# Kernel optimization log

Measured on AMD Instinct MI355X. Metric: run time of the kernel, lower is better.

## Reference

```python
import jax, jax.numpy as jnp
import numpy as np

B, T, D_IN, HID, D_OUT = 16, 4096, 256, 512, 256


def setup_inputs() -> dict:
    key = jax.random.key(0)
    k0, k1, k2, k3 = jax.random.split(key, 4)
    x = jax.random.normal(k0, (B, T, D_IN), dtype=jnp.float32)
    # nn.Linear default init ~ U(-1/sqrt(fan_in), 1/sqrt(fan_in)); approximate with scaled normal
    W_in = jax.random.normal(k1, (HID, D_IN), dtype=jnp.float32) / np.sqrt(D_IN)
    # hidden_ff.weight is explicitly set to diag(rand(hid_dim)) in the module
    W_h = jnp.diag(jax.random.uniform(k2, (HID,), dtype=jnp.float32))
    W_out = jax.random.normal(k3, (D_OUT, HID), dtype=jnp.float32) / np.sqrt(HID)
    return {"x": x, "W_in": W_in, "W_h": W_h, "W_out": W_out}


def reference(x, W_in, W_h, W_out):
    # x: [B, T, D_in]; W_in: [H, D_in]; W_h: [H, H]; W_out: [D_out, H]
    xp = jnp.einsum('btd,hd->bth', x, W_in)  # input projection, [B, T, H]

    def step(h, xt):
        # h_t = x_t + h_{t-1} @ W_h^T  (linear recurrence, h_0 = 0)
        h_next = xt + h @ W_h.T
        return h_next, h_next

    h0 = jnp.zeros((x.shape[0], W_h.shape[0]), dtype=x.dtype)
    _, hs = jax.lax.scan(step, h0, jnp.swapaxes(xp, 0, 1))  # hs: [T, B, H]
    hs = jnp.swapaxes(hs, 0, 1)  # [B, T, H]
    return jnp.einsum('bth,oh->bto', hs, W_out)  # [B, T, D_out]
```

## Files before the change

kernel.cpp:

```cpp
#include <hip/hip_runtime.h>
#include <hip/hip_bf16.h>
#include <stdint.h>

#define BATCH 16
#define SEQT  4096
#define DIN   256
#define HID   512
#define DOUT  256
#define M_TOT 65536
#define CLEN  128
#define NCHUNK 32

typedef short bf16x8 __attribute__((ext_vector_type(8)));
typedef float f32x4  __attribute__((ext_vector_type(4)));
typedef unsigned short u16;
typedef unsigned short u16x4 __attribute__((ext_vector_type(4)));
typedef unsigned int uint32;

__device__ __forceinline__ void ld_lds16(const void* g, void* l) {
    __builtin_amdgcn_global_load_lds(
        (const __attribute__((address_space(1))) void*)g,
        (__attribute__((address_space(3))) void*)l, 16, 0, 0);
}

__device__ __forceinline__ u16 f2bf_rne(float f) {
    uint32 v = __float_as_uint(f);
    v += 0x7FFFu + ((v >> 16) & 1u);
    return (u16)(v >> 16);
}

__device__ __forceinline__ void splitf(float f, u16& hi, u16& lo) {
    const uint32 u = __float_as_uint(f);
    hi = (u16)(u >> 16);
    lo = f2bf_rne(f - __uint_as_float(u & 0xFFFF0000u));
}

__global__ __launch_bounds__(256) void prep(
        const float* __restrict__ Wh, const float* __restrict__ Win,
        const float* __restrict__ Wout, float* __restrict__ wdiag,
        float* __restrict__ wpow, u16* __restrict__ Winhi,
        u16* __restrict__ Winlo, u16* __restrict__ Wouthi,
        u16* __restrict__ Woutlo) {
    const int bid = blockIdx.x, tid = threadIdx.x;
    if (bid == 0) {
        for (int h = tid; h < HID; h += 256) {
            const float wv = Wh[(size_t)h * HID + h];
            wdiag[h] = wv;
            float p = 1.f;
            for (int t = 0; t < CLEN; ++t) { p *= wv; wpow[t * HID + h] = p; }
        }
    } else if (bid <= 128) {
        const int f4 = (bid - 1) * 256 + tid;
        const f32x4 v = *(const f32x4*)(Win + (size_t)f4 * 4);
        u16x4 hv, lv;
#pragma unroll
        for (int k = 0; k < 4; ++k) { u16 a, b; splitf(v[k], a, b); hv[k] = a; lv[k] = b; }
        *(u16x4*)(Winhi + (size_t)f4 * 4) = hv;
        *(u16x4*)(Winlo + (size_t)f4 * 4) = lv;
    } else {
        const int f4 = (bid - 129) * 256 + tid;
        const f32x4 v = *(const f32x4*)(Wout + (size_t)f4 * 4);
        u16x4 hv, lv;
#pragma unroll
        for (int k = 0; k < 4; ++k) { u16 a, b; splitf(v[k], a, b); hv[k] = a; lv[k] = b; }
        *(u16x4*)(Wouthi + (size_t)f4 * 4) = hv;
        *(u16x4*)(Woutlo + (size_t)f4 * 4) = lv;
    }
}

__global__ __launch_bounds__(256, 2) void gemm1_scan(
        const float* __restrict__ X, const u16* __restrict__ Whi,
        const u16* __restrict__ Wlo, float* __restrict__ localo,
        float* __restrict__ L, const float* __restrict__ wdiag,
        const float* __restrict__ wpow) {
    __shared__ __align__(16) char smem[75776];
    u16*   Ah = (u16*)smem;
    u16*   Al = (u16*)(smem + 16384);
    u16*   Bh = (u16*)(smem + 32768);
    u16*   Bl = (u16*)(smem + 49152);
    float* st = (float*)smem;
    float* segT = (float*)(smem + 67584);
    float* segC = (float*)(smem + 71680);

    const int tid  = threadIdx.x;
    const int w    = tid >> 6;
    const int lane = tid & 63;

    const int bid  = blockIdx.x;
    const int xcd  = bid & 7;
    const int slot = bid >> 3;
    const int mBase = (xcd * 64 + (slot >> 2)) * 128;
    const int nBase = (slot & 3) * 128;

    const int wr = w >> 1, wc = w & 1;
    const int fr = lane & 15;
    const int kg = lane >> 4;

    const int bRow = lane >> 3;
    const int bCol = ((lane & 7) ^ bRow) * 8;

    f32x4 acc[4][4];
#pragma unroll
    for (int i = 0; i < 4; ++i)
#pragma unroll
        for (int j = 0; j < 4; ++j) acc[i][j] = (f32x4){0.f, 0.f, 0.f, 0.f};

    for (int k0 = 0; k0 < DIN; k0 += 64) {
#pragma unroll
        for (int i = 0; i < 4; ++i) {
            const int c = w * 4 + i;
            const int r = c * 8 + bRow;
            ld_lds16(Whi + (size_t)(nBase + r) * DIN + k0 + bCol, Bh + c * 512);
            ld_lds16(Wlo + (size_t)(nBase + r) * DIN + k0 + bCol, Bl + c * 512);
        }
#pragma unroll
        for (int it = 0; it < 4; ++it) {
            const int idx = it * 256 + tid;
            const int r  = idx >> 3;
            const int gl = idx & 7;
            const float* src = X + (size_t)(mBase + r) * DIN + k0 + gl * 8;
            const f32x4 v0 = *(const f32x4*)(src);
            const f32x4 v1 = *(const f32x4*)(src + 4);
            bf16x8 h8, l8;
#pragma unroll
            for (int e = 0; e < 4; ++e) {
                u16 a, b;
                splitf(v0[e], a, b); h8[e] = (short)a; l8[e] = (short)b;
                splitf(v1[e], a, b); h8[e + 4] = (short)a; l8[e + 4] = (short)b;
            }
            const int phys = r * 64 + ((gl ^ (r & 7)) * 8);
            *(bf16x8*)(Ah + phys) = h8;
            *(bf16x8*)(Al + phys) = l8;
        }
        __syncthreads();
#pragma unroll
        for (int ks = 0; ks < 2; ++ks) {
            const int colE = ks * 32 + kg * 8;
            bf16x8 ah[4], al[4], bh[4], bl[4];
#pragma unroll
            for (int f = 0; f < 4; ++f) {
                const int ra = wr * 64 + f * 16 + fr;
                const int pa = ra * 64 + (colE ^ ((fr & 7) << 3));
                ah[f] = *(const bf16x8*)(Ah + pa);
                al[f] = *(const bf16x8*)(Al + pa);
                const int rb = wc * 64 + f * 16 + fr;
                const int pb = rb * 64 + (colE ^ ((fr & 7) << 3));
                bh[f] = *(const bf16x8*)(Bh + pb);
                bl[f] = *(const bf16x8*)(Bl + pb);
            }
#pragma unroll
            for (int i = 0; i < 4; ++i)
#pragma unroll
                for (int j = 0; j < 4; ++j) {
                    acc[i][j] = __builtin_amdgcn_mfma_f32_16x16x32_bf16(ah[i], bh[j], acc[i][j], 0, 0, 0);
                    acc[i][j] = __builtin_amdgcn_mfma_f32_16x16x32_bf16(ah[i], bl[j], acc[i][j], 0, 0, 0);
                    acc[i][j] = __builtin_amdgcn_mfma_f32_16x16x32_bf16(al[i], bh[j], acc[i][j], 0, 0, 0);
                }
        }
        __syncthreads();
    }

#pragma unroll
    for (int i = 0; i < 4; ++i)
#pragma unroll
        for (int j = 0; j < 4; ++j)
#pragma unroll
            for (int rg = 0; rg < 4; ++rg)
                st[(wr * 64 + i * 16 + kg * 4 + rg) * 132 + wc * 64 + j * 16 + fr]
                    = acc[i][j][rg];
    __syncthreads();

    const int hcol = tid & 127;
    const int sh   = tid >> 7;
    const float wv = wdiag[nBase + hcol];
    float rr[4][16];
#pragma unroll
    for (int s = 0; s < 4; ++s) {
        float run = 0.f;
#pragma unroll
        for (int i = 0; i < 16; ++i) {
            run = fmaf(wv, run, st[((sh * 4 + s) * 16 + i) * 132 + hcol]);
            rr[s][i] = run;
        }
        segT[(sh * 4 + s) * 128 + hcol] = run;
    }
    __syncthreads();
    if (tid < 128) {
        const float w16 = wpow[15 * HID + nBase + tid];
        float c = 0.f;
#pragma unroll
        for (int s = 0; s < 8; ++s) {
            segC[s * 128 + tid] = c;
            c = fmaf(w16, c, segT[s * 128 + tid]);
        }
        const int cI = (mBase >> 7) & (NCHUNK - 1);
        const int bI = mBase >> 12;
        L[(cI * BATCH + bI) * HID + nBase + tid] = c;
    }
    __syncthreads();
#pragma unroll
    for (int s = 0; s < 4; ++s) {
        const float cin = segC[(sh * 4 + s) * 128 + hcol];
        float p = wv;
        float* dst = localo + (size_t)(mBase + (sh * 4 + s) * 16) * HID + nBase + hcol;
#pragma unroll
        for (int i = 0; i < 16; ++i) {
            dst[(size_t)i * HID] = fmaf(p, cin, rr[s][i]);
            p *= wv;
        }
    }
}

__global__ __launch_bounds__(256) void scan_carry(
        const float* __restrict__ L, const float* __restrict__ wpow,
        float* __restrict__ carry) {
    const int idx = blockIdx.x * 256 + threadIdx.x;
    const int h = idx & (HID - 1);
    const int b = idx >> 9;
    const float wf = wpow[(CLEN - 1) * HID + h];
    float H = 0.f;
    for (int c = 0; c < NCHUNK; ++c) {
        const int o = (c * BATCH + b) * HID + h;
        carry[o] = H;
        H = fmaf(wf, H, L[o]);
    }
}

__global__ __launch_bounds__(256, 2) void gemm2_fix(
        const float* __restrict__ localo, const u16* __restrict__ Bhi_g,
        const u16* __restrict__ Blo_g, const float* __restrict__ wpow,
        const float* __restrict__ carry, float* __restrict__ C) {
    __shared__ __align__(16) char smem[65536];
    u16* Ah = (u16*)smem;
    u16* Al = (u16*)(smem + 16384);
    u16* Bh = (u16*)(smem + 32768);
    u16* Bl = (u16*)(smem + 49152);

    const int tid  = threadIdx.x;
    const int w    = tid >> 6;
    const int lane = tid & 63;

    const int bid  = blockIdx.x;
    const int xcd  = bid & 7;
    const int slot = bid >> 3;
    const int mBase = (xcd * 64 + (slot >> 1)) * 128;
    const int nBase = (slot & 1) * 128;

    const int wr = w >> 1, wc = w & 1;
    const int fr = lane & 15;
    const int kg = lane >> 4;

    const int bRow = lane >> 3;
    const int bCol = ((lane & 7) ^ bRow) * 8;

    const int cI = (mBase >> 7) & (NCHUNK - 1);
    const int bI = mBase >> 12;
    const float* crow = carry + (size_t)(cI * BATCH + bI) * HID;

    f32x4 acc[4][4];
#pragma unroll
    for (int i = 0; i < 4; ++i)
#pragma unroll
        for (int j = 0; j < 4; ++j) acc[i][j] = (f32x4){0.f, 0.f, 0.f, 0.f};

    for (int k0 = 0; k0 < HID; k0 += 64) {
#pragma unroll
        for (int i = 0; i < 4; ++i) {
            const int c = w * 4 + i;
            const int r2 = c * 8 + bRow;
            ld_lds16(Bhi_g + (size_t)(nBase + r2) * HID + k0 + bCol, Bh + c * 512);
            ld_lds16(Blo_g + (size_t)(nBase + r2) * HID + k0 + bCol, Bl + c * 512);
        }
#pragma unroll
        for (int it = 0; it < 4; ++it) {
            const int idx = it * 256 + tid;
            const int r  = idx >> 3;
            const int gl = idx & 7;
            const int gm = mBase + r;
            const int tl = gm & (CLEN - 1);
            const size_t col = (size_t)(k0 + gl * 8);
            f32x4 v0 = *(const f32x4*)(localo + (size_t)gm * HID + col);
            f32x4 v1 = *(const f32x4*)(localo + (size_t)gm * HID + col + 4);
            const f32x4 p0 = *(const f32x4*)(wpow + (size_t)tl * HID + col);
            const f32x4 p1 = *(const f32x4*)(wpow + (size_t)tl * HID + col + 4);
            const f32x4 c0 = *(const f32x4*)(crow + col);
            const f32x4 c1 = *(const f32x4*)(crow + col + 4);
            bf16x8 h8, l8;
#pragma unroll
            for (int e = 0; e < 4; ++e) {
                const float f0 = fmaf(p0[e], c0[e], v0[e]);
                const float f1 = fmaf(p1[e], c1[e], v1[e]);
                u16 a, b;
                splitf(f0, a, b); h8[e] = (short)a; l8[e] = (short)b;
                splitf(f1, a, b); h8[e + 4] = (short)a; l8[e + 4] = (short)b;
            }
            const int phys = r * 64 + ((gl ^ (r & 7)) * 8);
            *(bf16x8*)(Ah + phys) = h8;
            *(bf16x8*)(Al + phys) = l8;
        }
        __syncthreads();
#pragma unroll
        for (int ks = 0; ks < 2; ++ks) {
            const int colE = ks * 32 + kg * 8;
            bf16x8 ah[4], al[4], bh[4], bl[4];
#pragma unroll
            for (int f = 0; f < 4; ++f) {
                const int ra = wr * 64 + f * 16 + fr;
                const int pa = ra * 64 + (colE ^ ((fr & 7) << 3));
                ah[f] = *(const bf16x8*)(Ah + pa);
                al[f] = *(const bf16x8*)(Al + pa);
                const int rb = wc * 64 + f * 16 + fr;
                const int pb = rb * 64 + (colE ^ ((fr & 7) << 3));
                bh[f] = *(const bf16x8*)(Bh + pb);
                bl[f] = *(const bf16x8*)(Bl + pb);
            }
#pragma unroll
            for (int i = 0; i < 4; ++i)
#pragma unroll
                for (int j = 0; j < 4; ++j) {
                    acc[i][j] = __builtin_amdgcn_mfma_f32_16x16x32_bf16(ah[i], bh[j], acc[i][j], 0, 0, 0);
                    acc[i][j] = __builtin_amdgcn_mfma_f32_16x16x32_bf16(ah[i], bl[j], acc[i][j], 0, 0, 0);
                    acc[i][j] = __builtin_amdgcn_mfma_f32_16x16x32_bf16(al[i], bh[j], acc[i][j], 0, 0, 0);
                }
        }
        __syncthreads();
    }

#pragma unroll
    for (int i = 0; i < 4; ++i) {
        const size_t row0 = (size_t)mBase + wr * 64 + i * 16 + kg * 4;
#pragma unroll
        for (int j = 0; j < 4; ++j) {
            const int col = nBase + wc * 64 + j * 16 + fr;
#pragma unroll
            for (int rg = 0; rg < 4; ++rg)
                C[(row0 + rg) * DOUT + col] = acc[i][j][rg];
        }
    }
}

extern "C" void kernel_launch(void* const* d_in, const int* in_sizes, int n_in,
                              void* d_out, int out_size, void* d_ws, size_t ws_size,
                              hipStream_t stream) {
    const float* x     = (const float*)d_in[0];
    const float* W_in  = (const float*)d_in[1];
    const float* W_h   = (const float*)d_in[2];
    const float* W_out = (const float*)d_in[3];
    float* out = (float*)d_out;

    char* ws = (char*)d_ws;
    float* localo = (float*)(ws);
    float* L      = (float*)(ws + 134217728);
    float* carry  = (float*)(ws + 135266304);
    float* wpow   = (float*)(ws + 136314880);
    float* wdiag  = (float*)(ws + 136577024);
    u16*   Winhi  = (u16*)(ws + 136579072);
    u16*   Winlo  = (u16*)(ws + 136841216);
    u16*   Wouthi = (u16*)(ws + 137103360);
    u16*   Woutlo = (u16*)(ws + 137365504);

    prep<<<257, 256, 0, stream>>>(W_h, W_in, W_out, wdiag, wpow,
                                  Winhi, Winlo, Wouthi, Woutlo);
    gemm1_scan<<<2048, 256, 0, stream>>>(x, Winhi, Winlo, localo, L, wdiag, wpow);
    scan_carry<<<32, 256, 0, stream>>>(L, wpow, carry);
    gemm2_fix<<<1024, 256, 0, stream>>>(localo, Wouthi, Woutlo, wpow, carry, out);
}
```

Baseline: 142.3 us.

## Shrink LDS tiles, pack hi/lo in one buffer, and scan in registers via shuffles

The K step is halved to 32 so the A and B tiles each hold the bf16 hi and lo halves in one 64-element row. B loads read Winlo and Woutlo through a fixed WHALF offset from the hi pointer. This cuts LDS use enough to raise launch bounds to 4 blocks per CU. The in-block recurrence scan in gemm1 now runs directly on MFMA accumulator registers using wave shuffles and precomputed powers of the decay, replacing the LDS staging pass and scalar scans. The risks are more barriers per K, since there are twice as many iterations, and the correctness of the new scan and of the offset-based lo addressing.

```diff
diff --git a/kernel.cpp b/kernel.cpp
--- a/kernel.cpp
+++ b/kernel.cpp
@@ -10,6 +10,7 @@
 #define M_TOT 65536
 #define CLEN  128
 #define NCHUNK 32
+#define WHALF 131072
 
 typedef short bf16x8 __attribute__((ext_vector_type(8)));
 typedef float f32x4  __attribute__((ext_vector_type(4)));
@@ -68,19 +69,13 @@
     }
 }
 
-__global__ __launch_bounds__(256, 2) void gemm1_scan(
+__global__ __launch_bounds__(256, 4) void gemm1_scan(
         const float* __restrict__ X, const u16* __restrict__ Whi,
-        const u16* __restrict__ Wlo, float* __restrict__ localo,
-        float* __restrict__ L, const float* __restrict__ wdiag,
-        const float* __restrict__ wpow) {
-    __shared__ __align__(16) char smem[75776];
-    u16*   Ah = (u16*)smem;
-    u16*   Al = (u16*)(smem + 16384);
-    u16*   Bh = (u16*)(smem + 32768);
-    u16*   Bl = (u16*)(smem + 49152);
-    float* st = (float*)smem;
-    float* segT = (float*)(smem + 67584);
-    float* segC = (float*)(smem + 71680);
+        float* __restrict__ localo, float* __restrict__ L,
+        const float* __restrict__ wdiag) {
+    __shared__ __align__(16) u16 Asm[128 * 64];
+    __shared__ __align__(16) u16 Bsm[128 * 64];
+    __shared__ float xw[128];
 
     const int tid  = threadIdx.x;
     const int w    = tid >> 6;
@@ -96,8 +91,10 @@
     const int fr = lane & 15;
     const int kg = lane >> 4;
 
-    const int bRow = lane >> 3;
-    const int bCol = ((lane & 7) ^ bRow) * 8;
+    const int bR = lane >> 3;
+    const int bP = lane & 7;
+    const int bLg = bP ^ bR;
+    const size_t bSrcOff = (size_t)(bLg >> 2) * WHALF + (size_t)(bLg & 3) * 8;
 
     f32x4 acc[4][4];
 #pragma unroll
@@ -105,108 +102,137 @@
 #pragma unroll
         for (int j = 0; j < 4; ++j) acc[i][j] = (f32x4){0.f, 0.f, 0.f, 0.f};
 
-    for (int k0 = 0; k0 < DIN; k0 += 64) {
+    const int ar = tid >> 1;
+    const int ahf = tid & 1;
+    const int arx = ar & 7;
+
+    for (int k0 = 0; k0 < DIN; k0 += 32) {
 #pragma unroll
         for (int i = 0; i < 4; ++i) {
             const int c = w * 4 + i;
-            const int r = c * 8 + bRow;
-            ld_lds16(Whi + (size_t)(nBase + r) * DIN + k0 + bCol, Bh + c * 512);
-            ld_lds16(Wlo + (size_t)(nBase + r) * DIN + k0 + bCol, Bl + c * 512);
-        }
-#pragma unroll
-        for (int it = 0; it < 4; ++it) {
-            const int idx = it * 256 + tid;
-            const int r  = idx >> 3;
-            const int gl = idx & 7;
-            const float* src = X + (size_t)(mBase + r) * DIN + k0 + gl * 8;
+            const int r = c * 8 + bR;
+            ld_lds16(Whi + bSrcOff + (size_t)(nBase + r) * DIN + k0,
+                     Bsm + c * 512);
+        }
+        {
+            const float* src = X + (size_t)(mBase + ar) * DIN + k0 + ahf * 16;
             const f32x4 v0 = *(const f32x4*)(src);
             const f32x4 v1 = *(const f32x4*)(src + 4);
-            bf16x8 h8, l8;
+            const f32x4 v2 = *(const f32x4*)(src + 8);
+            const f32x4 v3 = *(const f32x4*)(src + 12);
+            bf16x8 h0, l0, h1, l1;
 #pragma unroll
             for (int e = 0; e < 4; ++e) {
                 u16 a, b;
-                splitf(v0[e], a, b); h8[e] = (short)a; l8[e] = (short)b;
-                splitf(v1[e], a, b); h8[e + 4] = (short)a; l8[e + 4] = (short)b;
-            }
-            const int phys = r * 64 + ((gl ^ (r & 7)) * 8);
-            *(bf16x8*)(Ah + phys) = h8;
-            *(bf16x8*)(Al + phys) = l8;
+                splitf(v0[e], a, b); h0[e] = (short)a; l0[e] = (short)b;
+                splitf(v1[e], a, b); h0[e + 4] = (short)a; l0[e + 4] = (short)b;
+                splitf(v2[e], a, b); h1[e] = (short)a; l1[e] = (short)b;
+                splitf(v3[e], a, b); h1[e + 4] = (short)a; l1[e + 4] = (short)b;
+            }
+            const int g0 = ahf * 2, g1 = ahf * 2 + 1;
+            u16* arow = Asm + ar * 64;
+            *(bf16x8*)(arow + ((g0 ^ arx) * 8))       = h0;
+            *(bf16x8*)(arow + ((g1 ^ arx) * 8))       = h1;
+            *(bf16x8*)(arow + (((g0 + 4) ^ arx) * 8)) = l0;
+            *(bf16x8*)(arow + (((g1 + 4) ^ arx) * 8)) = l1;
         }
         __syncthreads();
-#pragma unroll
-        for (int ks = 0; ks < 2; ++ks) {
-            const int colE = ks * 32 + kg * 8;
-            bf16x8 ah[4], al[4], bh[4], bl[4];
-#pragma unroll
-            for (int f = 0; f < 4; ++f) {
-                const int ra = wr * 64 + f * 16 + fr;
-                const int pa = ra * 64 + (colE ^ ((fr & 7) << 3));
-                ah[f] = *(const bf16x8*)(Ah + pa);
-                al[f] = *(const bf16x8*)(Al + pa);
-                const int rb = wc * 64 + f * 16 + fr;
-                const int pb = rb * 64 + (colE ^ ((fr & 7) << 3));
-                bh[f] = *(const bf16x8*)(Bh + pb);
-                bl[f] = *(const bf16x8*)(Bl + pb);
-            }
-#pragma unroll
-            for (int i = 0; i < 4; ++i)
-#pragma unroll
-                for (int j = 0; j < 4; ++j) {
-                    acc[i][j] = __builtin_amdgcn_mfma_f32_16x16x32_bf16(ah[i], bh[j], acc[i][j], 0, 0, 0);
-                    acc[i][j] = __builtin_amdgcn_mfma_f32_16x16x32_bf16(ah[i], bl[j], acc[i][j], 0, 0, 0);
-                    acc[i][j] = __builtin_amdgcn_mfma_f32_16x16x32_bf16(al[i], bh[j], acc[i][j], 0, 0, 0);
-                }
-        }
+
+        bf16x8 ah[4], al[4], bh[4], bl[4];
+        const int rx = fr & 7;
+#pragma unroll
+        for (int f = 0; f < 4; ++f) {
+            const int sa = (wr * 64 + f * 16 + fr) * 64;
+            ah[f] = *(const bf16x8*)(Asm + sa + ((kg ^ rx) * 8));
+            al[f] = *(const bf16x8*)(Asm + sa + (((kg + 4) ^ rx) * 8));
+            const int sb = (wc * 64 + f * 16 + fr) * 64;
+            bh[f] = *(const bf16x8*)(Bsm + sb + ((kg ^ rx) * 8));
+            bl[f] = *(const bf16x8*)(Bsm + sb + (((kg + 4) ^ rx) * 8));
+        }
+#pragma unroll
+        for (int i = 0; i < 4; ++i)
+#pragma unroll
+            for (int j = 0; j < 4; ++j) {
+                acc[i][j] = __builtin_amdgcn_mfma_f32_16x16x32_bf16(ah[i], bh[j], acc[i][j], 0, 0, 0);
+                acc[i][j] = __builtin_amdgcn_mfma_f32_16x16x32_bf16(ah[i], bl[j], acc[i][j], 0, 0, 0);
+                acc[i][j] = __builtin_amdgcn_mfma_f32_16x16x32_bf16(al[i], bh[j], acc[i][j], 0, 0, 0);
+            }
         __syncthreads();
     }
 
-#pragma unroll
-    for (int i = 0; i < 4; ++i)
-#pragma unroll
-        for (int j = 0; j < 4; ++j)
-#pragma unroll
-            for (int rg = 0; rg < 4; ++rg)
-                st[(wr * 64 + i * 16 + kg * 4 + rg) * 132 + wc * 64 + j * 16 + fr]
-                    = acc[i][j][rg];
+    float w1[4], w2[4], w3[4], w4[4], w8[4], w16[4];
+#pragma unroll
+    for (int j = 0; j < 4; ++j) {
+        const float wv = wdiag[nBase + wc * 64 + j * 16 + fr];
+        w1[j] = wv; w2[j] = wv * wv; w3[j] = w2[j] * wv; w4[j] = w2[j] * w2[j];
+        w8[j] = w4[j] * w4[j]; w16[j] = w8[j] * w8[j];
+    }
+    float Bst[4] = {0.f, 0.f, 0.f, 0.f};
+#pragma unroll
+    for (int i = 0; i < 4; ++i) {
+#pragma unroll
+        for (int j = 0; j < 4; ++j) {
+            const float l0 = acc[i][j][0];
+            const float l1 = fmaf(w1[j], l0, acc[i][j][1]);
+            const float l2 = fmaf(w1[j], l1, acc[i][j][2]);
+            const float l3 = fmaf(w1[j], l2, acc[i][j][3]);
+            const float x0 = __shfl(l3, fr);
+            const float x1 = __shfl(l3, fr + 16);
+            const float x2 = __shfl(l3, fr + 32);
+            const float x3 = __shfl(l3, fr + 48);
+            float s = Bst[j];
+            float S = s;
+            s = fmaf(w4[j], s, x0); S = (kg == 1) ? s : S;
+            s = fmaf(w4[j], s, x1); S = (kg == 2) ? s : S;
+            s = fmaf(w4[j], s, x2); S = (kg == 3) ? s : S;
+            s = fmaf(w4[j], s, x3);
+            Bst[j] = s;
+            acc[i][j][0] = fmaf(w1[j], S, l0);
+            acc[i][j][1] = fmaf(w2[j], S, l1);
+            acc[i][j][2] = fmaf(w3[j], S, l2);
+            acc[i][j][3] = fmaf(w4[j], S, l3);
+        }
+    }
+    if (wr == 0 && kg == 0) {
+#pragma unroll
+        for (int j = 0; j < 4; ++j) xw[wc * 64 + j * 16 + fr] = Bst[j];
+    }
     __syncthreads();
-
-    const int hcol = tid & 127;
-    const int sh   = tid >> 7;
-    const float wv = wdiag[nBase + hcol];
-    float rr[4][16];
-#pragma unroll
-    for (int s = 0; s < 4; ++s) {
-        float run = 0.f;
-#pragma unroll
-        for (int i = 0; i < 16; ++i) {
-            run = fmaf(wv, run, st[((sh * 4 + s) * 16 + i) * 132 + hcol]);
-            rr[s][i] = run;
-        }
-        segT[(sh * 4 + s) * 128 + hcol] = run;
-    }
-    __syncthreads();
-    if (tid < 128) {
-        const float w16 = wpow[15 * HID + nBase + tid];
-        float c = 0.f;
-#pragma unroll
-        for (int s = 0; s < 8; ++s) {
-            segC[s * 128 + tid] = c;
-            c = fmaf(w16, c, segT[s * 128 + tid]);
-        }
+    if (wr == 1) {
         const int cI = (mBase >> 7) & (NCHUNK - 1);
         const int bI = mBase >> 12;
-        L[(cI * BATCH + bI) * HID + nBase + tid] = c;
-    }
-    __syncthreads();
-#pragma unroll
-    for (int s = 0; s < 4; ++s) {
-        const float cin = segC[(sh * 4 + s) * 128 + hcol];
-        float p = wv;
-        float* dst = localo + (size_t)(mBase + (sh * 4 + s) * 16) * HID + nBase + hcol;
-#pragma unroll
-        for (int i = 0; i < 16; ++i) {
-            dst[(size_t)i * HID] = fmaf(p, cin, rr[s][i]);
-            p *= wv;
+#pragma unroll
+        for (int j = 0; j < 4; ++j) {
+            const float cin = xw[wc * 64 + j * 16 + fr];
+            float wkg = 1.f;
+            if (kg & 1) wkg *= w4[j];
+            if (kg & 2) wkg *= w8[j];
+            float f = wkg;
+#pragma unroll
+            for (int i = 0; i < 4; ++i) {
+                const float g = f * cin;
+                acc[i][j][0] = fmaf(w1[j], g, acc[i][j][0]);
+                acc[i][j][1] = fmaf(w2[j], g, acc[i][j][1]);
+                acc[i][j][2] = fmaf(w3[j], g, acc[i][j][2]);
+                acc[i][j][3] = fmaf(w4[j], g, acc[i][j][3]);
+                f *= w16[j];
+            }
+            if (kg == 0) {
+                const float w32 = w16[j] * w16[j];
+                const float w64 = w32 * w32;
+                L[(cI * BATCH + bI) * HID + nBase + wc * 64 + j * 16 + fr]
+                    = fmaf(w64, cin, Bst[j]);
+            }
+        }
+    }
+#pragma unroll
+    for (int i = 0; i < 4; ++i) {
+        const size_t row0 = (size_t)(mBase + wr * 64 + i * 16 + kg * 4);
+#pragma unroll
+        for (int rg = 0; rg < 4; ++rg) {
+            float* dst = localo + (row0 + rg) * HID + nBase + wc * 64 + fr;
+#pragma unroll
+            for (int j = 0; j < 4; ++j) dst[j * 16] = acc[i][j][rg];
         }
     }
 }
@@ -226,15 +252,12 @@
     }
 }
 
-__global__ __launch_bounds__(256, 2) void gemm2_fix(
+__global__ __launch_bounds__(256, 4) void gemm2_fix(
         const float* __restrict__ localo, const u16* __restrict__ Bhi_g,
-        const u16* __restrict__ Blo_g, const float* __restrict__ wpow,
-        const float* __restrict__ carry, float* __restrict__ C) {
-    __shared__ __align__(16) char smem[65536];
-    u16* Ah = (u16*)smem;
-    u16* Al = (u16*)(smem + 16384);
-    u16* Bh = (u16*)(smem + 32768);
-    u16* Bl = (u16*)(smem + 49152);
+        const float* __restrict__ wpow, const float* __restrict__ carry,
+        float* __restrict__ C) {
+    __shared__ __align__(16) u16 Asm[128 * 64];
+    __shared__ __align__(16) u16 Bsm[128 * 64];
 
     const int tid  = threadIdx.x;
     const int w    = tid >> 6;
@@ -250,79 +273,86 @@
     const int fr = lane & 15;
     const int kg = lane >> 4;
 
-    const int bRow = lane >> 3;
-    const int bCol = ((lane & 7) ^ bRow) * 8;
+    const int bR = lane >> 3;
+    const int bP = lane & 7;
+    const int bLg = bP ^ bR;
+    const size_t bSrcOff = (size_t)(bLg >> 2) * WHALF + (size_t)(bLg & 3) * 8;
 
     const int cI = (mBase >> 7) & (NCHUNK - 1);
     const int bI = mBase >> 12;
     const float* crow = carry + (size_t)(cI * BATCH + bI) * HID;
 
+    const int ar = tid >> 1;
+    const int ahf = tid & 1;
+    const int arx = ar & 7;
+
     f32x4 acc[4][4];
 #pragma unroll
     for (int i = 0; i < 4; ++i)
 #pragma unroll
         for (int j = 0; j < 4; ++j) acc[i][j] = (f32x4){0.f, 0.f, 0.f, 0.f};
 
-    for (int k0 = 0; k0 < HID; k0 += 64) {
+    for (int k0 = 0; k0 < HID; k0 += 32) {
 #pragma unroll
         for (int i = 0; i < 4; ++i) {
             const int c = w * 4 + i;
-            const int r2 = c * 8 + bRow;
-            ld_lds16(Bhi_g + (size_t)(nBase + r2) * HID + k0 + bCol, Bh + c * 512);
-            ld_lds16(Blo_g + (size_t)(nBase + r2) * HID + k0 + bCol, Bl + c * 512);
-        }
-#pragma unroll
-        for (int it = 0; it < 4; ++it) {
-            const int idx = it * 256 + tid;
-            const int r  = idx >> 3;
-            const int gl = idx & 7;
-            const int gm = mBase + r;
-            const int tl = gm & (CLEN - 1);
-            const size_t col = (size_t)(k0 + gl * 8);
-            f32x4 v0 = *(const f32x4*)(localo + (size_t)gm * HID + col);
-            f32x4 v1 = *(const f32x4*)(localo + (size_t)gm * HID + col + 4);
-            const f32x4 p0 = *(const f32x4*)(wpow + (size_t)tl * HID + col);
-            const f32x4 p1 = *(const f32x4*)(wpow + (size_t)tl * HID + col + 4);
-            const f32x4 c0 = *(const f32x4*)(crow + col);
-            const f32x4 c1 = *(const f32x4*)(crow + col + 4);
-            bf16x8 h8, l8;
-#pragma unroll
-            for (int e = 0; e < 4; ++e) {
-                const float f0 = fmaf(p0[e], c0[e], v0[e]);
-                const float f1 = fmaf(p1[e], c1[e], v1[e]);
-                u16 a, b;
-                splitf(f0, a, b); h8[e] = (short)a; l8[e] = (short)b;
-                splitf(f1, a, b); h8[e + 4] = (short)a; l8[e + 4] = (short)b;
-            }
-            const int phys = r * 64 + ((gl ^ (r & 7)) * 8);
-            *(bf16x8*)(Ah + phys) = h8;
-            *(bf16x8*)(Al + phys) = l8;
+            const int r = c * 8 + bR;
+            ld_lds16(Bhi_g + bSrcOff + (size_t)(nBase + r) * HID + k0,
+                     Bsm + c * 512);
+        }
+        {
+            const size_t col = (size_t)(k0 + ahf * 16);
+            const float* vsrc = localo + (size_t)(mBase + ar) * HID + col;
+            const float* psrc = wpow + (size_t)ar * HID + col;
+            const float* csrc = crow + col;
+            bf16x8 h0, l0, h1, l1;
+#pragma unroll
+            for (int q = 0; q < 2; ++q) {
+                const f32x4 va = *(const f32x4*)(vsrc + q * 8);
+                const f32x4 vb = *(const f32x4*)(vsrc + q * 8 + 4);
+                const f32x4 pa = *(const f32x4*)(psrc + q * 8);
+                const f32x4 pb = *(const f32x4*)(psrc + q * 8 + 4);
+                const f32x4 ca = *(const f32x4*)(csrc + q * 8);
+                const f32x4 cb = *(const f32x4*)(csrc + q * 8 + 4);
+                bf16x8 h8, l8;
+#pragma unroll
+                for (int e = 0; e < 4; ++e) {
+                    const float f0 = fmaf(pa[e], ca[e], va[e]);
+                    const float f1 = fmaf(pb[e], cb[e], vb[e]);
+                    u16 a, b;
+                    splitf(f0, a, b); h8[e] = (short)a; l8[e] = (short)b;
+                    splitf(f1, a, b); h8[e + 4] = (short)a; l8[e + 4] = (short)b;
+                }
+                if (q == 0) { h0 = h8; l0 = l8; } else { h1 = h8; l1 = l8; }
+            }
+            const int g0 = ahf * 2, g1 = ahf * 2 + 1;
+            u16* arow = Asm + ar * 64;
+            *(bf16x8*)(arow + ((g0 ^ arx) * 8))       = h0;
+            *(bf16x8*)(arow + ((g1 ^ arx) * 8))       = h1;
+            *(bf16x8*)(arow + (((g0 + 4) ^ arx) * 8)) = l0;
+            *(bf16x8*)(arow + (((g1 + 4) ^ arx) * 8)) = l1;
         }
         __syncthreads();
-#pragma unroll
-        for (int ks = 0; ks < 2; ++ks) {
-            const int colE = ks * 32 + kg * 8;
-            bf16x8 ah[4], al[4], bh[4], bl[4];
-#pragma unroll
-            for (int f = 0; f < 4; ++f) {
-                const int ra = wr * 64 + f * 16 + fr;
-                const int pa = ra * 64 + (colE ^ ((fr & 7) << 3));
-                ah[f] = *(const bf16x8*)(Ah + pa);
-                al[f] = *(const bf16x8*)(Al + pa);
-                const int rb = wc * 64 + f * 16 + fr;
-                const int pb = rb * 64 + (colE ^ ((fr & 7) << 3));
-                bh[f] = *(const bf16x8*)(Bh + pb);
-                bl[f] = *(const bf16x8*)(Bl + pb);
-            }
-#pragma unroll
-            for (int i = 0; i < 4; ++i)
-#pragma unroll
-                for (int j = 0; j < 4; ++j) {
-                    acc[i][j] = __builtin_amdgcn_mfma_f32_16x16x32_bf16(ah[i], bh[j], acc[i][j], 0, 0, 0);
-                    acc[i][j] = __builtin_amdgcn_mfma_f32_16x16x32_bf16(ah[i], bl[j], acc[i][j], 0, 0, 0);
-                    acc[i][j] = __builtin_amdgcn_mfma_f32_16x16x32_bf16(al[i], bh[j], acc[i][j], 0, 0, 0);
-                }
-        }
+
+        bf16x8 ah[4], al[4], bh[4], bl[4];
+        const int rx = fr & 7;
+#pragma unroll
+        for (int f = 0; f < 4; ++f) {
+            const int sa = (wr * 64 + f * 16 + fr) * 64;
+            ah[f] = *(const bf16x8*)(Asm + sa + ((kg ^ rx) * 8));
+            al[f] = *(const bf16x8*)(Asm + sa + (((kg + 4) ^ rx) * 8));
+            const int sb = (wc * 64 + f * 16 + fr) * 64;
+            bh[f] = *(const bf16x8*)(Bsm + sb + ((kg ^ rx) * 8));
+            bl[f] = *(const bf16x8*)(Bsm + sb + (((kg + 4) ^ rx) * 8));
+        }
+#pragma unroll
+        for (int i = 0; i < 4; ++i)
+#pragma unroll
+            for (int j = 0; j < 4; ++j) {
+                acc[i][j] = __builtin_amdgcn_mfma_f32_16x16x32_bf16(ah[i], bh[j], acc[i][j], 0, 0, 0);
+                acc[i][j] = __builtin_amdgcn_mfma_f32_16x16x32_bf16(ah[i], bl[j], acc[i][j], 0, 0, 0);
+                acc[i][j] = __builtin_amdgcn_mfma_f32_16x16x32_bf16(al[i], bh[j], acc[i][j], 0, 0, 0);
+            }
         __syncthreads();
     }
 
@@ -361,7 +391,7 @@
 
     prep<<<257, 256, 0, stream>>>(W_h, W_in, W_out, wdiag, wpow,
                                   Winhi, Winlo, Wouthi, Woutlo);
-    gemm1_scan<<<2048, 256, 0, stream>>>(x, Winhi, Winlo, localo, L, wdiag, wpow);
+    gemm1_scan<<<2048, 256, 0, stream>>>(x, Winhi, localo, L, wdiag);
     scan_carry<<<32, 256, 0, stream>>>(L, wpow, carry);
-    gemm2_fix<<<1024, 256, 0, stream>>>(localo, Wouthi, Woutlo, wpow, carry, out);
-}
+    gemm2_fix<<<1024, 256, 0, stream>>>(localo, Wouthi, wpow, carry, out);
+}
```

Result: slower. 202.8 us (+42.5%).
